# Kernel optimization log

Hardware: AMD Instinct MI355X
Metric: run time of the kernel (lower is better)

Reference implementation:

```python
import jax, jax.numpy as jnp
import numpy as np

EPS = 1e-6


def _att_vector(x, W, b, sharp2, th2, is_last):
    """AttentionVector on a 2D payoff slice.
    x: (N, a, m). W: (1, 2), b: (1,). Returns (N, a)."""
    # compare_param: pair (x[n,j,k], x[n,i,k]) -> Linear(2,1) -> sigmoid -> mean over k
    # Linear on the concat pair is w00*x[n,j,k] + w01*x[n,i,k] + b, so we fuse it.
    lin = W[0, 0] * x[:, None, :, :] + W[0, 1] * x[:, :, None, :] + b[0]  # (N,a,a,m)
    c = jnp.mean(jax.nn.sigmoid(lin), axis=3)  # (N,a,a)
    # max_normalize over dim 2
    c = c / (jnp.max(c, axis=2, keepdims=True) + EPS)
    # compute_player_mask
    m = jnp.mean(c, axis=2)  # (N,a)
    m = jax.nn.relu(m * sharp2[0] + th2[0])
    m = jax.nn.softmax(m, axis=1)
    if not is_last:
        m = m / (jnp.max(m, axis=1, keepdims=True) + EPS)
    return m


def setup_inputs() -> dict:
    key = jax.random.key(0)
    ks = jax.random.split(key, 16)
    N, a1, a2, f = 128, 64, 64, 2
    inp = {
        "x": jax.random.normal(ks[0], (N, f, a1, a2), dtype=jnp.float32),
        "fc_W": jax.random.normal(ks[1], (2, 2), dtype=jnp.float32) * 0.5,
        "fc_b": jax.random.normal(ks[2], (2,), dtype=jnp.float32) * 0.1,
        "p1_W": jax.random.normal(ks[3], (1, 2), dtype=jnp.float32) * 0.5,
        "p1_b": jax.random.normal(ks[4], (1,), dtype=jnp.float32) * 0.1,
        "p1_sharp": jnp.ones((1,), dtype=jnp.float32),
        "p1_th": jnp.zeros((1,), dtype=jnp.float32),
        "p2_W": jax.random.normal(ks[5], (1, 2), dtype=jnp.float32) * 0.5,
        "p2_b": jax.random.normal(ks[6], (1,), dtype=jnp.float32) * 0.1,
        "p2_sharp": jnp.ones((1,), dtype=jnp.float32),
        "p2_th": jnp.zeros((1,), dtype=jnp.float32),
        "out_W": jax.random.normal(ks[7], (1, 2), dtype=jnp.float32) * 0.5,
        "out_b": jax.random.normal(ks[8], (1,), dtype=jnp.float32) * 0.1,
        "out_sharp": jnp.ones((1,), dtype=jnp.float32),
        "out_th": jnp.zeros((1,), dtype=jnp.float32),
    }
    return inp


def reference(x, fc_W, fc_b, p1_W, p1_b, p1_sharp, p1_th,
              p2_W, p2_b, p2_sharp, p2_th,
              out_W, out_b, out_sharp, out_th):
    # x: (N, f=2, a1, a2) -> (N, a1, a2, f)
    h = jnp.transpose(x, (0, 2, 3, 1))
    # is_fc_first: Linear(2, 2) + ReLU on last dim
    h = jax.nn.relu(h @ fc_W.T + fc_b)  # (N,a1,a2,2)
    # one AttentionModule (module_layers=1, not simult)
    vec1 = _att_vector(h[..., 0], p1_W, p1_b, p1_sharp, p1_th, is_last=False)  # (N,a1)
    h = h * vec1[:, :, None, None]
    pl2 = jnp.transpose(h[..., 1], (0, 2, 1))  # (N,a2,a1)
    vec2 = _att_vector(pl2, p2_W, p2_b, p2_sharp, p2_th, is_last=False)  # (N,a2)
    h = h * vec2[:, None, :, None]
    # with_last: final AttentionVector (is_last=True) on player-1 channel
    out = _att_vector(h[..., 0], out_W, out_b, out_sharp, out_th, is_last=True)  # (N,a1)
    return out
```

## Files before the change

kernel.cpp:

```cpp
#include <hip/hip_runtime.h>


constexpr int A   = 64;
constexpr int PAD = 68;
constexpr float L2E  = 1.4426950408889634f;
constexpr float EPSF = 1e-6f;

__device__ __forceinline__ float bcast(float v, int srcLane) {
    return __int_as_float(__builtin_amdgcn_readlane(__float_as_int(v), srcLane));
}
__device__ __forceinline__ float rcpf(float v) { return __builtin_amdgcn_rcpf(v); }
__device__ __forceinline__ float ex2(float v)  { return __builtin_amdgcn_exp2f(v); }

template <int CTRL>
__device__ __forceinline__ float upd_dpp(float src) {
    return __int_as_float(__builtin_amdgcn_update_dpp(
        0, __float_as_int(src), CTRL, 0xF, 0xF, true));
}
__device__ __forceinline__ float wave_sum64(float x) {
    x += upd_dpp<0x111>(x);
    x += upd_dpp<0x112>(x);
    x += upd_dpp<0x114>(x);
    x += upd_dpp<0x118>(x);
    x += upd_dpp<0x142>(x);
    x += upd_dpp<0x143>(x);
    return bcast(x, 63);
}
__device__ __forceinline__ float wave_max64(float x) {
    x = fmaxf(x, upd_dpp<0x111>(x));
    x = fmaxf(x, upd_dpp<0x112>(x));
    x = fmaxf(x, upd_dpp<0x114>(x));
    x = fmaxf(x, upd_dpp<0x118>(x));
    x = fmaxf(x, upd_dpp<0x142>(x));
    x = fmaxf(x, upd_dpp<0x143>(x));
    return bcast(x, 63);
}

__device__ __forceinline__ void att2q(const float* __restrict__ prow,
                                      const float* __restrict__ qL,
                                      int row0, int lane,
                                      float* __restrict__ mg)
{
    const float qreg0 = qL[row0 * PAD + lane];
    const float qreg1 = qL[(row0 + 1) * PAD + lane];
    float acc0 = 0.f, acc1 = 0.f;
#pragma unroll 1
    for (int c = 0; c < 4; ++c) {
        float pk[16];
        *(float4*)(&pk[0])  = *(const float4*)(prow + c * 16 + 0);
        *(float4*)(&pk[4])  = *(const float4*)(prow + c * 16 + 4);
        *(float4*)(&pk[8])  = *(const float4*)(prow + c * 16 + 8);
        *(float4*)(&pk[12]) = *(const float4*)(prow + c * 16 + 12);
#pragma unroll
        for (int t = 0; t < 8; ++t) {
            const int k0 = c * 16 + 2 * t, k1 = k0 + 1;
            {
                float u0 = fmaf(pk[2 * t],     bcast(qreg0, k0), 1.0f);
                float u1 = fmaf(pk[2 * t + 1], bcast(qreg0, k1), 1.0f);
                acc0 = fmaf(u0 + u1, rcpf(u0 * u1), acc0);
            }
            {
                float u0 = fmaf(pk[2 * t],     bcast(qreg1, k0), 1.0f);
                float u1 = fmaf(pk[2 * t + 1], bcast(qreg1, k1), 1.0f);
                acc1 = fmaf(u0 + u1, rcpf(u0 * u1), acc1);
            }
        }
    }
    const float s0 = wave_sum64(acc0), m0 = wave_max64(acc0);
    const float s1 = wave_sum64(acc1), m1 = wave_max64(acc1);
    if (lane == 0) {
        float v0 = (s0 * (1.0f / 4096.0f)) / (m0 * (1.0f / 64.0f) + EPSF);
        float v1 = (s1 * (1.0f / 4096.0f)) / (m1 * (1.0f / 64.0f) + EPSF);
        __hip_atomic_store(mg + row0,     v0 + 2.0f, __ATOMIC_RELAXED, __HIP_MEMORY_SCOPE_AGENT);
        __hip_atomic_store(mg + row0 + 1, v1 + 2.0f, __ATOMIC_RELAXED, __HIP_MEMORY_SCOPE_AGENT);
    }
}

__device__ __forceinline__ float poll_all(const float* __restrict__ mg, int lane)
{
    for (;;) {
        float f = __hip_atomic_load(mg + lane, __ATOMIC_RELAXED, __HIP_MEMORY_SCOPE_AGENT);
        unsigned u = __float_as_uint(f);
        if (__all((u >> 23) == 0x80u)) return f - 2.0f;
        __builtin_amdgcn_s_sleep(1);
    }
}

__device__ __forceinline__ float softmax64(float m, float sharp, float th, bool last)
{
    float v = fmaxf(0.f, m * sharp + th);
    float mx = wave_max64(v);
    float e = __expf(v - mx);
    float s = wave_sum64(e);
    float r = e / s;
    if (!last) {
        float rm = wave_max64(r);
        r = r / (rm + EPSF);
    }
    return r;
}

__device__ __forceinline__ float gather4(float v, int wv, int lane)
{
    float r0 = bcast(v, 4 * wv + 0);
    float r1 = bcast(v, 4 * wv + 1);
    float r2 = bcast(v, 4 * wv + 2);
    float r3 = bcast(v, 4 * wv + 3);
    int g = (lane >> 4) & 3;
    float lo = (g & 1) ? r1 : r0;
    float hi = (g & 1) ? r3 : r2;
    return (g & 2) ? hi : lo;
}

__global__ __launch_bounds__(1024, 4)
void attn_half(const float* __restrict__ x,
               const float* __restrict__ fcW, const float* __restrict__ fcb,
               const float* __restrict__ p1W, const float* __restrict__ p1b,
               const float* __restrict__ p1s, const float* __restrict__ p1t,
               const float* __restrict__ p2W, const float* __restrict__ p2b,
               const float* __restrict__ p2s, const float* __restrict__ p2t,
               const float* __restrict__ oW,  const float* __restrict__ ob,
               const float* __restrict__ os,  const float* __restrict__ ot,
               float* __restrict__ mglob,
               float* __restrict__ out)
{
    __shared__ __align__(16) float pL[A * PAD];
    __shared__ __align__(16) float qL[A * PAD];

    const int tid = threadIdx.x, lane = tid & 63, wv = tid >> 6;
    const int n = blockIdx.x >> 1, half = blockIdx.x & 1;
    const int row0 = half * 32 + wv * 2;
    const int i = tid >> 4, j = (tid & 15) * 4;
    float* mg = mglob + (size_t)n * 3 * A;

    const float4* x0v = (const float4*)(x + (size_t)n * 2 * A * A);
    const float4* x1v = x0v + (A * A / 4);
    const float4 a = x0v[tid];
    const float4 c = x1v[tid];
    const float w00 = fcW[0], w01 = fcW[1], w10 = fcW[2], w11 = fcW[3];
    const float b0 = fcb[0], b1 = fcb[1];
    const float h0v[4] = { fmaxf(0.f, w00 * a.x + w01 * c.x + b0),
                           fmaxf(0.f, w00 * a.y + w01 * c.y + b0),
                           fmaxf(0.f, w00 * a.z + w01 * c.z + b0),
                           fmaxf(0.f, w00 * a.w + w01 * c.w + b0) };
    const float h1v[4] = { fmaxf(0.f, w10 * a.x + w11 * c.x + b1),
                           fmaxf(0.f, w10 * a.y + w11 * c.y + b1),
                           fmaxf(0.f, w10 * a.z + w11 * c.z + b1),
                           fmaxf(0.f, w10 * a.w + w11 * c.w + b1) };

    {
        const float W0 = p1W[0], W1 = p1W[1], bb = p1b[0];
        float4 pv, qv;
        pv.x = ex2(-L2E * (W0 * h0v[0] + bb)); qv.x = ex2(-L2E * (W1 * h0v[0]));
        pv.y = ex2(-L2E * (W0 * h0v[1] + bb)); qv.y = ex2(-L2E * (W1 * h0v[1]));
        pv.z = ex2(-L2E * (W0 * h0v[2] + bb)); qv.z = ex2(-L2E * (W1 * h0v[2]));
        pv.w = ex2(-L2E * (W0 * h0v[3] + bb)); qv.w = ex2(-L2E * (W1 * h0v[3]));
        *(float4*)&pL[i * PAD + j] = pv;
        *(float4*)&qL[i * PAD + j] = qv;
    }
    __syncthreads();
    att2q(pL + lane * PAD, qL, row0, lane, mg);
    const float v1reg = softmax64(poll_all(mg, lane), p1s[0], p1t[0], false);
    __syncthreads();

    const float sc1 = gather4(v1reg, wv, lane);
    {
        const float W0 = p2W[0], W1 = p2W[1], bb = p2b[0];
#pragma unroll
        for (int t = 0; t < 4; ++t) {
            float hv = h1v[t] * sc1;
            pL[(j + t) * PAD + i] = ex2(-L2E * (W0 * hv + bb));
            qL[(j + t) * PAD + i] = ex2(-L2E * (W1 * hv));
        }
    }
    __syncthreads();
    att2q(pL + lane * PAD, qL, row0, lane, mg + A);
    const float v2reg = softmax64(poll_all(mg + A, lane), p2s[0], p2t[0], false);
    __syncthreads();

    {
        const float W0 = oW[0], W1 = oW[1], bb = ob[0];
        float pv[4], qv[4];
#pragma unroll
        for (int t = 0; t < 4; ++t) {
            float v2t = __shfl(v2reg, j + t, 64);
            float hv = h0v[t] * sc1 * v2t;
            pv[t] = ex2(-L2E * (W0 * hv + bb));
            qv[t] = ex2(-L2E * (W1 * hv));
        }
        *(float4*)&pL[i * PAD + j] = *(float4*)&pv[0];
        *(float4*)&qL[i * PAD + j] = *(float4*)&qv[0];
    }
    __syncthreads();
    att2q(pL + lane * PAD, qL, row0, lane, mg + 2 * A);

    if (half == 0 && wv == 0) {
        float r = softmax64(poll_all(mg + 2 * A, lane), os[0], ot[0], true);
        out[(size_t)n * A + lane] = r;
    }
}

extern "C" void kernel_launch(void* const* d_in, const int* in_sizes, int n_in,
                              void* d_out, int out_size, void* d_ws, size_t ws_size,
                              hipStream_t stream)
{
    (void)n_in; (void)out_size; (void)ws_size;
    const float* x   = (const float*)d_in[0];
    const float* fcW = (const float*)d_in[1];
    const float* fcb = (const float*)d_in[2];
    const float* p1W = (const float*)d_in[3];
    const float* p1b = (const float*)d_in[4];
    const float* p1s = (const float*)d_in[5];
    const float* p1t = (const float*)d_in[6];
    const float* p2W = (const float*)d_in[7];
    const float* p2b = (const float*)d_in[8];
    const float* p2s = (const float*)d_in[9];
    const float* p2t = (const float*)d_in[10];
    const float* oW  = (const float*)d_in[11];
    const float* ob  = (const float*)d_in[12];
    const float* os  = (const float*)d_in[13];
    const float* ot  = (const float*)d_in[14];
    float* out = (float*)d_out;

    const int N = in_sizes[0] / (2 * A * A);
    float* mglob = (float*)d_ws;

    attn_half<<<2 * N, 1024, 0, stream>>>(x, fcW, fcb,
                                          p1W, p1b, p1s, p1t,
                                          p2W, p2b, p2s, p2t,
                                          oW, ob, os, ot, mglob, out);
}
```

Baseline: 106.3 us.

## Exchange half-block results via LDS with one polling wave, batch reciprocals

```diff
diff --git a/kernel.cpp b/kernel.cpp
--- a/kernel.cpp
+++ b/kernel.cpp
@@ -39,12 +39,13 @@
 __device__ __forceinline__ void att2q(const float* __restrict__ prow,
                                       const float* __restrict__ qL,
                                       int row0, int lane,
+                                      float* __restrict__ mbuf,
                                       float* __restrict__ mg)
 {
     const float qreg0 = qL[row0 * PAD + lane];
     const float qreg1 = qL[(row0 + 1) * PAD + lane];
     float acc0 = 0.f, acc1 = 0.f;
-#pragma unroll 1
+#pragma unroll
     for (int c = 0; c < 4; ++c) {
         float pk[16];
         *(float4*)(&pk[0])  = *(const float4*)(prow + c * 16 + 0);
@@ -52,17 +53,27 @@
         *(float4*)(&pk[8])  = *(const float4*)(prow + c * 16 + 8);
         *(float4*)(&pk[12]) = *(const float4*)(prow + c * 16 + 12);
 #pragma unroll
-        for (int t = 0; t < 8; ++t) {
-            const int k0 = c * 16 + 2 * t, k1 = k0 + 1;
+        for (int g = 0; g < 4; ++g) {
+            const int k = c * 16 + 4 * g;
+            const float p0 = pk[4 * g], p1 = pk[4 * g + 1];
+            const float p2 = pk[4 * g + 2], p3 = pk[4 * g + 3];
             {
-                float u0 = fmaf(pk[2 * t],     bcast(qreg0, k0), 1.0f);
-                float u1 = fmaf(pk[2 * t + 1], bcast(qreg0, k1), 1.0f);
-                acc0 = fmaf(u0 + u1, rcpf(u0 * u1), acc0);
+                float u0 = fmaf(p0, bcast(qreg0, k),     1.0f);
+                float u1 = fmaf(p1, bcast(qreg0, k + 1), 1.0f);
+                float u2 = fmaf(p2, bcast(qreg0, k + 2), 1.0f);
+                float u3 = fmaf(p3, bcast(qreg0, k + 3), 1.0f);
+                float a = u0 * u1, b = u2 * u3;
+                float numer = fmaf(u0 + u1, b, (u2 + u3) * a);
+                acc0 = fmaf(numer, rcpf(a * b), acc0);
             }
             {
-                float u0 = fmaf(pk[2 * t],     bcast(qreg1, k0), 1.0f);
-                float u1 = fmaf(pk[2 * t + 1], bcast(qreg1, k1), 1.0f);
-                acc1 = fmaf(u0 + u1, rcpf(u0 * u1), acc1);
+                float u0 = fmaf(p0, bcast(qreg1, k),     1.0f);
+                float u1 = fmaf(p1, bcast(qreg1, k + 1), 1.0f);
+                float u2 = fmaf(p2, bcast(qreg1, k + 2), 1.0f);
+                float u3 = fmaf(p3, bcast(qreg1, k + 3), 1.0f);
+                float a = u0 * u1, b = u2 * u3;
+                float numer = fmaf(u0 + u1, b, (u2 + u3) * a);
+                acc1 = fmaf(numer, rcpf(a * b), acc1);
             }
         }
     }
@@ -71,18 +82,10 @@
     if (lane == 0) {
         float v0 = (s0 * (1.0f / 4096.0f)) / (m0 * (1.0f / 64.0f) + EPSF);
         float v1 = (s1 * (1.0f / 4096.0f)) / (m1 * (1.0f / 64.0f) + EPSF);
+        mbuf[row0]     = v0;
+        mbuf[row0 + 1] = v1;
         __hip_atomic_store(mg + row0,     v0 + 2.0f, __ATOMIC_RELAXED, __HIP_MEMORY_SCOPE_AGENT);
         __hip_atomic_store(mg + row0 + 1, v1 + 2.0f, __ATOMIC_RELAXED, __HIP_MEMORY_SCOPE_AGENT);
-    }
-}
-
-__device__ __forceinline__ float poll_all(const float* __restrict__ mg, int lane)
-{
-    for (;;) {
-        float f = __hip_atomic_load(mg + lane, __ATOMIC_RELAXED, __HIP_MEMORY_SCOPE_AGENT);
-        unsigned u = __float_as_uint(f);
-        if (__all((u >> 23) == 0x80u)) return f - 2.0f;
-        __builtin_amdgcn_s_sleep(1);
     }
 }
 
@@ -98,6 +101,23 @@
         r = r / (rm + EPSF);
     }
     return r;
+}
+
+__device__ __forceinline__ void pull_peer(float* __restrict__ mbuf,
+                                          const float* __restrict__ mg,
+                                          int half, int lane)
+{
+    if ((lane >> 5) != half) {
+        const float* p = mg + lane;
+        float f;
+        for (;;) {
+            f = __hip_atomic_load(p, __ATOMIC_RELAXED, __HIP_MEMORY_SCOPE_AGENT);
+            unsigned u = __float_as_uint(f);
+            if ((u >> 23) == 0x80u) break;
+            __builtin_amdgcn_s_sleep(1);
+        }
+        mbuf[lane] = f - 2.0f;
+    }
 }
 
 __device__ __forceinline__ float gather4(float v, int wv, int lane)
@@ -126,6 +146,7 @@
 {
     __shared__ __align__(16) float pL[A * PAD];
     __shared__ __align__(16) float qL[A * PAD];
+    __shared__ float mbuf[A];
 
     const int tid = threadIdx.x, lane = tid & 63, wv = tid >> 6;
     const int n = blockIdx.x >> 1, half = blockIdx.x & 1;
@@ -159,11 +180,12 @@
         *(float4*)&qL[i * PAD + j] = qv;
     }
     __syncthreads();
-    att2q(pL + lane * PAD, qL, row0, lane, mg);
-    const float v1reg = softmax64(poll_all(mg, lane), p1s[0], p1t[0], false);
-    __syncthreads();
-
+    att2q(pL + lane * PAD, qL, row0, lane, mbuf, mg);
+    if (wv == 15) pull_peer(mbuf, mg, half, lane);
+    __syncthreads();
+    const float v1reg = softmax64(mbuf[lane], p1s[0], p1t[0], false);
     const float sc1 = gather4(v1reg, wv, lane);
+
     {
         const float W0 = p2W[0], W1 = p2W[1], bb = p2b[0];
 #pragma unroll
@@ -174,9 +196,10 @@
         }
     }
     __syncthreads();
-    att2q(pL + lane * PAD, qL, row0, lane, mg + A);
-    const float v2reg = softmax64(poll_all(mg + A, lane), p2s[0], p2t[0], false);
-    __syncthreads();
+    att2q(pL + lane * PAD, qL, row0, lane, mbuf, mg + A);
+    if (wv == 15) pull_peer(mbuf, mg + A, half, lane);
+    __syncthreads();
+    const float v2reg = softmax64(mbuf[lane], p2s[0], p2t[0], false);
 
     {
         const float W0 = oW[0], W1 = oW[1], bb = ob[0];
@@ -192,11 +215,19 @@
         *(float4*)&qL[i * PAD + j] = *(float4*)&qv[0];
     }
     __syncthreads();
-    att2q(pL + lane * PAD, qL, row0, lane, mg + 2 * A);
-
-    if (half == 0 && wv == 0) {
-        float r = softmax64(poll_all(mg + 2 * A, lane), os[0], ot[0], true);
-        out[(size_t)n * A + lane] = r;
+    att2q(pL + lane * PAD, qL, row0, lane, mbuf, mg + 2 * A);
+
+    if (wv == 0) {
+        const float* p = mg + 2 * A + lane;
+        float f;
+        for (;;) {
+            f = __hip_atomic_load(p, __ATOMIC_RELAXED, __HIP_MEMORY_SCOPE_AGENT);
+            unsigned u = __float_as_uint(f);
+            if ((u >> 23) == 0x80u) break;
+            __builtin_amdgcn_s_sleep(1);
+        }
+        float r = softmax64(f - 2.0f, os[0], ot[0], true);
+        if ((lane >> 5) == half) out[(size_t)n * A + lane] = r;
     }
 }
 
```

New measurement: 101.5 us. -4.5%, faster.
